# Kernel tuning notes

Hardware: AMD Instinct MI355X
Metric: run time of the kernel (lower is better)

## Reference

```python
import jax, jax.numpy as jnp
import numpy as np

N = 50000
E = 800000
NODE_DIM = 128
EDGE_DIM = 64


def leaky_relu(x, slope=0.2):
    return jnp.where(x >= 0, x, slope * x)


def setup_inputs() -> dict:
    key = jax.random.key(0)
    ks = jax.random.split(key, 12)
    node_feats = jax.random.normal(ks[0], (N, NODE_DIM), dtype=jnp.float32)
    edge_index = jax.random.randint(ks[1], (2, E), 0, N, dtype=jnp.int64)
    edge_feats = jax.random.normal(ks[2], (E, EDGE_DIM), dtype=jnp.float32)
    # msg_mlp: Linear(node+edge -> node), LeakyReLU(0.2), Linear(node -> node)
    s1 = 1.0 / np.sqrt(NODE_DIM + EDGE_DIM)
    s2 = 1.0 / np.sqrt(NODE_DIM)
    s3 = 1.0 / np.sqrt(2 * NODE_DIM)
    msg_w1 = jax.random.uniform(ks[3], (NODE_DIM + EDGE_DIM, NODE_DIM), jnp.float32, -s1, s1)
    msg_b1 = jax.random.uniform(ks[4], (NODE_DIM,), jnp.float32, -s1, s1)
    msg_w2 = jax.random.uniform(ks[5], (NODE_DIM, NODE_DIM), jnp.float32, -s2, s2)
    msg_b2 = jax.random.uniform(ks[6], (NODE_DIM,), jnp.float32, -s2, s2)
    # update_mlp: Linear(2*node -> node), LeakyReLU(0.2), Linear(node -> node)
    upd_w1 = jax.random.uniform(ks[7], (2 * NODE_DIM, NODE_DIM), jnp.float32, -s3, s3)
    upd_b1 = jax.random.uniform(ks[8], (NODE_DIM,), jnp.float32, -s3, s3)
    upd_w2 = jax.random.uniform(ks[9], (NODE_DIM, NODE_DIM), jnp.float32, -s2, s2)
    upd_b2 = jax.random.uniform(ks[10], (NODE_DIM,), jnp.float32, -s2, s2)
    return {
        "node_feats": node_feats,
        "edge_feats": edge_feats,
        "msg_w1": msg_w1, "msg_b1": msg_b1, "msg_w2": msg_w2, "msg_b2": msg_b2,
        "upd_w1": upd_w1, "upd_b1": upd_b1, "upd_w2": upd_w2, "upd_b2": upd_b2,
        "edge_index": edge_index,
    }


def reference(node_feats, edge_feats, msg_w1, msg_b1, msg_w2, msg_b2,
              upd_w1, upd_b1, upd_w2, upd_b2, edge_index):
    src = edge_index[0]
    dst = edge_index[1]
    # gather neighbor features, concat with edge features: (E, node+edge)
    msg_input = jnp.concatenate([node_feats[dst], edge_feats], axis=1)
    h = leaky_relu(msg_input @ msg_w1 + msg_b1)
    messages = h @ msg_w2 + msg_b2                       # (E, node_dim)
    # scatter-add messages to source nodes
    aggregated = jax.ops.segment_sum(messages, src, num_segments=node_feats.shape[0])
    update_input = jnp.concatenate([node_feats, aggregated], axis=1)  # (N, 2*node_dim)
    h2 = leaky_relu(update_input @ upd_w1 + upd_b1)
    return h2 @ upd_w2 + upd_b2                          # (N, node_dim)
```

## Files before the change

kernel.cpp:

```cpp
#include <hip/hip_runtime.h>
#include <hip/hip_bf16.h>

#define NNODES 50000
#define NEDGES 800000
#define NDIM   128
#define EDIM   64
#define K1     192
#define K2     256
#define NB     196

#define KP1 200
#define KPA 136
#define KPU 264
#define MSTR 132

typedef __attribute__((ext_vector_type(8))) short bf16x8;
typedef __attribute__((ext_vector_type(4))) short bf16x4;
typedef __attribute__((ext_vector_type(4))) float f32x4;

__device__ inline short f2bf(float f) {
  union { float f; unsigned u; } v; v.f = f;
  unsigned r = v.u + 0x7FFFu + ((v.u >> 16) & 1u);
  return (short)(r >> 16);
}

__device__ inline bf16x4 pack4(float4 v) {
  bf16x4 p;
  p[0] = f2bf(v.x); p[1] = f2bf(v.y); p[2] = f2bf(v.z); p[3] = f2bf(v.w);
  return p;
}

__global__ __launch_bounds__(256) void cvt_kernel(const float* __restrict__ src,
                                                  short* __restrict__ dst, int n) {
  int i = (blockIdx.x * 256 + threadIdx.x) * 4;
  if (i < n) {
    float4 v = *(const float4*)(src + i);
    *(bf16x4*)(dst + i) = pack4(v);
  }
}

__global__ __launch_bounds__(256) void wt_kernel(const float* __restrict__ w,
                                                 short* __restrict__ wt, int K) {
  int i = blockIdx.x * 256 + threadIdx.x;
  if (i < K * NDIM) {
    int k = i >> 7;
    int n = i & 127;
    wt[n * K + k] = f2bf(w[i]);
  }
}

__global__ __launch_bounds__(256) void hist_kernel(const int* __restrict__ eidx,
                                                   int* __restrict__ cnt) {
  int i = blockIdx.x * 256 + threadIdx.x;
  if (i < NEDGES) atomicAdd(&cnt[eidx[i]], 1);
}

__global__ __launch_bounds__(256) void scan_reduce_kernel(const int* __restrict__ cnt,
                                                          int* __restrict__ bsum) {
  __shared__ int sh[256];
  int tid = threadIdx.x;
  int i = blockIdx.x * 256 + tid;
  sh[tid] = (i < NNODES) ? cnt[i] : 0;
  __syncthreads();
#pragma unroll
  for (int off = 128; off > 0; off >>= 1) {
    if (tid < off) sh[tid] += sh[tid + off];
    __syncthreads();
  }
  if (tid == 0) bsum[blockIdx.x] = sh[0];
}

__global__ __launch_bounds__(256) void scan_top_kernel(const int* __restrict__ bsum,
                                                       int* __restrict__ bscan) {
  __shared__ int sh[256];
  int tid = threadIdx.x;
  int v = (tid < NB) ? bsum[tid] : 0;
  sh[tid] = v;
  __syncthreads();
#pragma unroll
  for (int off = 1; off < 256; off <<= 1) {
    int t = (tid >= off) ? sh[tid - off] : 0;
    __syncthreads();
    sh[tid] += t;
    __syncthreads();
  }
  bscan[tid] = sh[tid] - v;
}

__global__ __launch_bounds__(256) void scan_down_kernel(int* __restrict__ cnt,
                                                        const int* __restrict__ bscan,
                                                        int* __restrict__ row_ptr) {
  __shared__ int sh[256];
  int tid = threadIdx.x;
  int i = blockIdx.x * 256 + tid;
  int v = (i < NNODES) ? cnt[i] : 0;
  sh[tid] = v;
  __syncthreads();
#pragma unroll
  for (int off = 1; off < 256; off <<= 1) {
    int t = (tid >= off) ? sh[tid - off] : 0;
    __syncthreads();
    sh[tid] += t;
    __syncthreads();
  }
  if (i < NNODES) {
    row_ptr[i] = bscan[blockIdx.x] + (sh[tid] - v);
    cnt[i] = 0;
  }
}

__global__ __launch_bounds__(256) void permute_kernel(const int* __restrict__ eidx,
                                                      const int* __restrict__ row_ptr,
                                                      int* __restrict__ cnt,
                                                      int4* __restrict__ s_edges) {
  int e = blockIdx.x * 256 + threadIdx.x;
  if (e < NEDGES) {
    int s = eidx[e];
    int d = eidx[NEDGES + e];
    int pos = row_ptr[s] + atomicAdd(&cnt[s], 1);
    s_edges[pos] = make_int4(s, d, e, 0);
  }
}

__global__ __launch_bounds__(256, 6) void edge_kernel(const short* __restrict__ nf_bf,
                                                      const float* __restrict__ edge_feats,
                                                      const int4* __restrict__ s_edges,
                                                      const short* __restrict__ w1t,
                                                      const float* __restrict__ b1,
                                                      float* __restrict__ hagg) {
  __shared__ __align__(16) char SH[64 * KP1 * 2];
  __shared__ int srcs[64];
  __shared__ int dsts[64];
  __shared__ int eids[64];

  short* X = (short*)SH;
  float* M = (float*)SH;

  const int tid = threadIdx.x;
  const int e0 = blockIdx.x * 64;

  if (tid < 64) {
    int4 v = s_edges[e0 + tid];
    srcs[tid] = v.x;
    dsts[tid] = v.y;
    eids[tid] = v.z;
  }
  __syncthreads();

  {
    int r = tid >> 2, q = tid & 3;
    const bf16x8* np = (const bf16x8*)(nf_bf + (size_t)dsts[r] * NDIM) + q * 4;
    const float4* ep = (const float4*)(edge_feats + (size_t)eids[r] * EDIM) + q * 4;
    short* dpn = X + r * KP1 + q * 32;
    short* dpe = X + r * KP1 + NDIM + q * 16;
#pragma unroll
    for (int j = 0; j < 4; ++j) *(bf16x8*)(dpn + j * 8) = np[j];
#pragma unroll
    for (int j = 0; j < 4; ++j) *(bf16x4*)(dpe + j * 4) = pack4(ep[j]);
  }
  __syncthreads();

  const int lane = tid & 63;
  const int wv = tid >> 6;
  const int m16 = lane & 15;
  const int quad = lane >> 4;

  f32x4 acc[4][2];
#pragma unroll
  for (int mt = 0; mt < 4; ++mt)
#pragma unroll
    for (int nt = 0; nt < 2; ++nt)
      acc[mt][nt] = (f32x4){0.f, 0.f, 0.f, 0.f};

#pragma unroll
  for (int ks = 0; ks < 6; ++ks) {
    const int k0 = ks * 32 + quad * 8;
    bf16x8 b[2];
#pragma unroll
    for (int nt = 0; nt < 2; ++nt) {
      int n = wv * 32 + nt * 16 + m16;
      b[nt] = *(const bf16x8*)(w1t + n * K1 + k0);
    }
#pragma unroll
    for (int mt = 0; mt < 4; ++mt) {
      bf16x8 a = *(const bf16x8*)(X + (mt * 16 + m16) * KP1 + k0);
#pragma unroll
      for (int nt = 0; nt < 2; ++nt)
        acc[mt][nt] = __builtin_amdgcn_mfma_f32_16x16x32_bf16(a, b[nt], acc[mt][nt], 0, 0, 0);
    }
  }
  __syncthreads();

#pragma unroll
  for (int h = 0; h < 2; ++h) {
#pragma unroll
    for (int nt = 0; nt < 2; ++nt) {
      int col = wv * 32 + nt * 16 + m16;
      float bb = b1[col];
#pragma unroll
      for (int mt2 = 0; mt2 < 2; ++mt2) {
        int mt = h * 2 + mt2;
#pragma unroll
        for (int i = 0; i < 4; ++i) {
          float v = acc[mt][nt][i] + bb;
          v = v >= 0.f ? v : 0.2f * v;
          int lr = mt2 * 16 + quad * 4 + i;
          M[lr * MSTR + col] = v;
        }
      }
    }
    __syncthreads();
    {
      const int c = tid & 127;
      const int lr0 = (tid >> 7) * 16;
      const int g0 = h * 32 + lr0;
      float a = M[lr0 * MSTR + c];
      int prev = srcs[g0];
#pragma unroll 4
      for (int r = 1; r < 16; ++r) {
        int s = srcs[g0 + r];
        float v = M[(lr0 + r) * MSTR + c];
        if (s != prev) {
          atomicAdd(&hagg[(size_t)prev * NDIM + c], a);
          a = v;
          prev = s;
        } else {
          a += v;
        }
      }
      atomicAdd(&hagg[(size_t)prev * NDIM + c], a);
    }
    if (h == 0) __syncthreads();
  }
}

__global__ __launch_bounds__(256) void node_kernel(const short* __restrict__ nf_bf,
                                                   const float* __restrict__ hagg,
                                                   const int* __restrict__ degc,
                                                   const short* __restrict__ w2t,
                                                   const float* __restrict__ b2,
                                                   const short* __restrict__ u1t,
                                                   const float* __restrict__ ub1,
                                                   const short* __restrict__ u2t,
                                                   const float* __restrict__ ub2,
                                                   float* __restrict__ out) {
  __shared__ __align__(16) short AGH[64 * KPA];
  __shared__ __align__(16) short XU[64 * KPU];
  __shared__ float degs[64];

  const int tid = threadIdx.x;
  const int n0 = blockIdx.x * 64;

  if (tid < 64) {
    int node = n0 + tid;
    degs[tid] = (node < NNODES) ? (float)degc[node] : 0.f;
  }
  {
    int r = tid >> 2, q = tid & 3;
    int node = n0 + r; if (node >= NNODES) node = NNODES - 1;
    const float4* hp = (const float4*)(hagg + (size_t)node * NDIM) + q * 8;
    const bf16x8* xp = (const bf16x8*)(nf_bf + (size_t)node * NDIM) + q * 4;
    short* ap = AGH + r * KPA + q * 32;
    short* xq = XU + r * KPU + q * 32;
#pragma unroll
    for (int j = 0; j < 8; ++j) *(bf16x4*)(ap + j * 4) = pack4(hp[j]);
#pragma unroll
    for (int j = 0; j < 4; ++j) *(bf16x8*)(xq + j * 8) = xp[j];
  }
  __syncthreads();

  const int lane = tid & 63;
  const int wv = tid >> 6;
  const int m16 = lane & 15;
  const int quad = lane >> 4;

  f32x4 acc[4][2];

#pragma unroll
  for (int mt = 0; mt < 4; ++mt)
#pragma unroll
    for (int nt = 0; nt < 2; ++nt)
      acc[mt][nt] = (f32x4){0.f, 0.f, 0.f, 0.f};
#pragma unroll
  for (int ks = 0; ks < 4; ++ks) {
    const int k0 = ks * 32 + quad * 8;
    bf16x8 b[2];
#pragma unroll
    for (int nt = 0; nt < 2; ++nt) {
      int n = wv * 32 + nt * 16 + m16;
      b[nt] = *(const bf16x8*)(w2t + n * NDIM + k0);
    }
#pragma unroll
    for (int mt = 0; mt < 4; ++mt) {
      bf16x8 a = *(const bf16x8*)(AGH + (mt * 16 + m16) * KPA + k0);
#pragma unroll
      for (int nt = 0; nt < 2; ++nt)
        acc[mt][nt] = __builtin_amdgcn_mfma_f32_16x16x32_bf16(a, b[nt], acc[mt][nt], 0, 0, 0);
    }
  }
#pragma unroll
  for (int nt = 0; nt < 2; ++nt) {
    int col = wv * 32 + nt * 16 + m16;
    float bb = b2[col];
#pragma unroll
    for (int mt = 0; mt < 4; ++mt) {
#pragma unroll
      for (int i = 0; i < 4; ++i) {
        int row = mt * 16 + quad * 4 + i;
        float v = acc[mt][nt][i] + degs[row] * bb;
        XU[row * KPU + NDIM + col] = f2bf(v);
      }
    }
  }
  __syncthreads();

#pragma unroll
  for (int mt = 0; mt < 4; ++mt)
#pragma unroll
    for (int nt = 0; nt < 2; ++nt)
      acc[mt][nt] = (f32x4){0.f, 0.f, 0.f, 0.f};
#pragma unroll
  for (int ks = 0; ks < 8; ++ks) {
    const int k0 = ks * 32 + quad * 8;
    bf16x8 b[2];
#pragma unroll
    for (int nt = 0; nt < 2; ++nt) {
      int n = wv * 32 + nt * 16 + m16;
      b[nt] = *(const bf16x8*)(u1t + n * K2 + k0);
    }
#pragma unroll
    for (int mt = 0; mt < 4; ++mt) {
      bf16x8 a = *(const bf16x8*)(XU + (mt * 16 + m16) * KPU + k0);
#pragma unroll
      for (int nt = 0; nt < 2; ++nt)
        acc[mt][nt] = __builtin_amdgcn_mfma_f32_16x16x32_bf16(a, b[nt], acc[mt][nt], 0, 0, 0);
    }
  }
  __syncthreads();
#pragma unroll
  for (int nt = 0; nt < 2; ++nt) {
    int col = wv * 32 + nt * 16 + m16;
    float bb = ub1[col];
#pragma unroll
    for (int mt = 0; mt < 4; ++mt) {
#pragma unroll
      for (int i = 0; i < 4; ++i) {
        int row = mt * 16 + quad * 4 + i;
        float v = acc[mt][nt][i] + bb;
        v = v >= 0.f ? v : 0.2f * v;
        AGH[row * KPA + col] = f2bf(v);
      }
    }
  }
  __syncthreads();

#pragma unroll
  for (int mt = 0; mt < 4; ++mt)
#pragma unroll
    for (int nt = 0; nt < 2; ++nt)
      acc[mt][nt] = (f32x4){0.f, 0.f, 0.f, 0.f};
#pragma unroll
  for (int ks = 0; ks < 4; ++ks) {
    const int k0 = ks * 32 + quad * 8;
    bf16x8 b[2];
#pragma unroll
    for (int nt = 0; nt < 2; ++nt) {
      int n = wv * 32 + nt * 16 + m16;
      b[nt] = *(const bf16x8*)(u2t + n * NDIM + k0);
    }
#pragma unroll
    for (int mt = 0; mt < 4; ++mt) {
      bf16x8 a = *(const bf16x8*)(AGH + (mt * 16 + m16) * KPA + k0);
#pragma unroll
      for (int nt = 0; nt < 2; ++nt)
        acc[mt][nt] = __builtin_amdgcn_mfma_f32_16x16x32_bf16(a, b[nt], acc[mt][nt], 0, 0, 0);
    }
  }
#pragma unroll
  for (int nt = 0; nt < 2; ++nt) {
    int col = wv * 32 + nt * 16 + m16;
    float bb = ub2[col];
#pragma unroll
    for (int mt = 0; mt < 4; ++mt) {
#pragma unroll
      for (int i = 0; i < 4; ++i) {
        int row = mt * 16 + quad * 4 + i;
        int node = n0 + row;
        if (node < NNODES)
          out[(size_t)node * NDIM + col] = acc[mt][nt][i] + bb;
      }
    }
  }
}

extern "C" void kernel_launch(void* const* d_in, const int* in_sizes, int n_in,
                              void* d_out, int out_size, void* d_ws, size_t ws_size,
                              hipStream_t stream) {
  const float* node_feats = (const float*)d_in[0];
  const float* edge_feats = (const float*)d_in[1];
  const float* msg_w1 = (const float*)d_in[2];
  const float* msg_b1 = (const float*)d_in[3];
  const float* msg_w2 = (const float*)d_in[4];
  const float* msg_b2 = (const float*)d_in[5];
  const float* upd_w1 = (const float*)d_in[6];
  const float* upd_b1 = (const float*)d_in[7];
  const float* upd_w2 = (const float*)d_in[8];
  const float* upd_b2 = (const float*)d_in[9];
  const int* eidx = (const int*)d_in[10];

  float* hagg   = (float*)d_ws;
  int* cnt      = (int*)(hagg + (size_t)NNODES * NDIM);
  int* row_ptr  = cnt + NNODES;
  int* bsum     = row_ptr + NNODES;
  int* bscan    = bsum + 256;
  int4* s_edges = (int4*)(bscan + 256);
  short* w1t    = (short*)(s_edges + NEDGES);
  short* w2t    = w1t + 128 * K1;
  short* u1t    = w2t + 128 * 128;
  short* u2t    = u1t + 128 * K2;
  short* nf_bf  = u2t + 128 * 128;

  hipMemsetAsync(d_ws, 0, (size_t)(NNODES * NDIM + NNODES) * sizeof(float), stream);

  cvt_kernel<<<(NNODES * NDIM / 4 + 255) / 256, 256, 0, stream>>>(node_feats, nf_bf,
                                                                  NNODES * NDIM);
  wt_kernel<<<(K1 * 128) / 256, 256, 0, stream>>>(msg_w1, w1t, K1);
  wt_kernel<<<(128 * 128) / 256, 256, 0, stream>>>(msg_w2, w2t, 128);
  wt_kernel<<<(K2 * 128) / 256, 256, 0, stream>>>(upd_w1, u1t, K2);
  wt_kernel<<<(128 * 128) / 256, 256, 0, stream>>>(upd_w2, u2t, 128);

  hist_kernel<<<NEDGES / 256, 256, 0, stream>>>(eidx, cnt);
  scan_reduce_kernel<<<NB, 256, 0, stream>>>(cnt, bsum);
  scan_top_kernel<<<1, 256, 0, stream>>>(bsum, bscan);
  scan_down_kernel<<<NB, 256, 0, stream>>>(cnt, bscan, row_ptr);
  permute_kernel<<<NEDGES / 256, 256, 0, stream>>>(eidx, row_ptr, cnt, s_edges);

  edge_kernel<<<NEDGES / 64, 256, 0, stream>>>(nf_bf, edge_feats, s_edges,
                                               w1t, msg_b1, hagg);
  node_kernel<<<(NNODES + 63) / 64, 256, 0, stream>>>(nf_bf, hagg, cnt,
                                                      w2t, msg_b2, u1t, upd_b1,
                                                      u2t, upd_b2, (float*)d_out);
}
```

Before: 541.7 us.

## Permute MFMA A-row mapping to segment-reduce edges in registers

Remaps which edge rows each MFMA tile loads so every lane's accumulator holds 16 consecutive edges of one output column. The bias, LeakyReLU and run-length segment reduction over sorted sources then happen directly in registers. This drops the LDS staging buffer M, its writes and reads, and several block barriers. The cost is larger per-thread register arrays, plus atomics issued from MFMA lanes whose 16-lane groups hit strided addresses rather than threads covering contiguous columns.

```diff
diff --git a/kernel.cpp b/kernel.cpp
--- a/kernel.cpp
+++ b/kernel.cpp
@@ -12,7 +12,6 @@
 #define KP1 200
 #define KPA 136
 #define KPU 264
-#define MSTR 132
 
 typedef __attribute__((ext_vector_type(8))) short bf16x8;
 typedef __attribute__((ext_vector_type(4))) short bf16x4;
@@ -128,13 +127,10 @@
                                                       const short* __restrict__ w1t,
                                                       const float* __restrict__ b1,
                                                       float* __restrict__ hagg) {
-  __shared__ __align__(16) char SH[64 * KP1 * 2];
+  __shared__ __align__(16) short X[64 * KP1];
   __shared__ int srcs[64];
   __shared__ int dsts[64];
   __shared__ int eids[64];
-
-  short* X = (short*)SH;
-  float* M = (float*)SH;
 
   const int tid = threadIdx.x;
   const int e0 = blockIdx.x * 64;
@@ -164,6 +160,7 @@
   const int wv = tid >> 6;
   const int m16 = lane & 15;
   const int quad = lane >> 4;
+  const int ar0 = ((m16 >> 2) << 4) + (m16 & 3);
 
   f32x4 acc[4][2];
 #pragma unroll
@@ -183,54 +180,40 @@
     }
 #pragma unroll
     for (int mt = 0; mt < 4; ++mt) {
-      bf16x8 a = *(const bf16x8*)(X + (mt * 16 + m16) * KP1 + k0);
+      bf16x8 a = *(const bf16x8*)(X + (ar0 + mt * 4) * KP1 + k0);
 #pragma unroll
       for (int nt = 0; nt < 2; ++nt)
         acc[mt][nt] = __builtin_amdgcn_mfma_f32_16x16x32_bf16(a, b[nt], acc[mt][nt], 0, 0, 0);
     }
   }
-  __syncthreads();
-
-#pragma unroll
-  for (int h = 0; h < 2; ++h) {
-#pragma unroll
-    for (int nt = 0; nt < 2; ++nt) {
-      int col = wv * 32 + nt * 16 + m16;
-      float bb = b1[col];
-#pragma unroll
-      for (int mt2 = 0; mt2 < 2; ++mt2) {
-        int mt = h * 2 + mt2;
-#pragma unroll
-        for (int i = 0; i < 4; ++i) {
-          float v = acc[mt][nt][i] + bb;
-          v = v >= 0.f ? v : 0.2f * v;
-          int lr = mt2 * 16 + quad * 4 + i;
-          M[lr * MSTR + col] = v;
-        }
+
+  const int rb = quad << 4;
+#pragma unroll
+  for (int nt = 0; nt < 2; ++nt) {
+    const int col = (wv << 5) + (nt << 4) + m16;
+    const float bb = b1[col];
+    float v[16];
+#pragma unroll
+    for (int mt = 0; mt < 4; ++mt)
+#pragma unroll
+      for (int i = 0; i < 4; ++i) {
+        float t = acc[mt][nt][i] + bb;
+        v[(mt << 2) + i] = t >= 0.f ? t : 0.2f * t;
       }
-    }
-    __syncthreads();
-    {
-      const int c = tid & 127;
-      const int lr0 = (tid >> 7) * 16;
-      const int g0 = h * 32 + lr0;
-      float a = M[lr0 * MSTR + c];
-      int prev = srcs[g0];
-#pragma unroll 4
-      for (int r = 1; r < 16; ++r) {
-        int s = srcs[g0 + r];
-        float v = M[(lr0 + r) * MSTR + c];
-        if (s != prev) {
-          atomicAdd(&hagg[(size_t)prev * NDIM + c], a);
-          a = v;
-          prev = s;
-        } else {
-          a += v;
-        }
+    float run = v[0];
+    int prev = srcs[rb];
+#pragma unroll
+    for (int r = 1; r < 16; ++r) {
+      int s = srcs[rb + r];
+      if (s != prev) {
+        atomicAdd(&hagg[(size_t)prev * NDIM + col], run);
+        run = v[r];
+        prev = s;
+      } else {
+        run += v[r];
       }
-      atomicAdd(&hagg[(size_t)prev * NDIM + c], a);
-    }
-    if (h == 0) __syncthreads();
+    }
+    atomicAdd(&hagg[(size_t)prev * NDIM + col], run);
   }
 }
 
```

Result: slower. 553.2 us (+2.1%).
